# Kernel optimization log

Measured on AMD Instinct MI355X. Metric: run time of the kernel, lower is better.

Reference implementation:

```python
import jax, jax.numpy as jnp
import numpy as np

D = 768
B, T = 4, 4096


def _layernorm(x, gamma, bias):
    # Faithful to the (buggy) original: (x - mu/sqrt(var)) * gamma + bias,
    # with torch's default unbiased variance (ddof=1).
    mu = jnp.mean(x, axis=-1, keepdims=True)
    var = jnp.var(x, axis=-1, keepdims=True, ddof=1)
    return (x - mu / jnp.sqrt(var)) * gamma + bias


def setup_inputs() -> dict:
    key = jax.random.key(0)
    ks = jax.random.split(key, 8)
    # kaiming_uniform_ default: bound = sqrt(6 / fan_in) with a=sqrt(5) -> gain = sqrt(2/(1+5)) = sqrt(1/3)
    # bound = gain * sqrt(3/fan_in) = sqrt(1/fan_in)
    bound_attn = 1.0 / np.sqrt(D)
    bound_lin = 1.0 / np.sqrt(D)  # torch Linear default init bound
    return {
        "x": jax.random.normal(ks[0], (B, T, D), dtype=jnp.float32),
        "ln1_g": jnp.ones((D,), jnp.float32),
        "ln1_b": jnp.zeros((D,), jnp.float32),
        "wq": jax.random.uniform(ks[1], (D, D), jnp.float32, -bound_attn, bound_attn),
        "wk": jax.random.uniform(ks[2], (D, D), jnp.float32, -bound_attn, bound_attn),
        "wv": jax.random.uniform(ks[3], (D, D), jnp.float32, -bound_attn, bound_attn),
        "ln2_g": jnp.ones((D,), jnp.float32),
        "ln2_b": jnp.zeros((D,), jnp.float32),
        "fc1_w": jax.random.uniform(ks[4], (D, D), jnp.float32, -bound_lin, bound_lin),
        "fc1_b": jax.random.uniform(ks[5], (D,), jnp.float32, -bound_lin, bound_lin),
        "fc2_w": jax.random.uniform(ks[6], (D, D), jnp.float32, -bound_lin, bound_lin),
        "fc2_b": jax.random.uniform(ks[7], (D,), jnp.float32, -bound_lin, bound_lin),
    }


def reference(x, ln1_g, ln1_b, wq, wk, wv, ln2_g, ln2_b, fc1_w, fc1_b, fc2_w, fc2_b):
    d_model = x.shape[-1]
    # LN 1
    y = _layernorm(x, ln1_g, ln1_b)
    # Naive single-head attention (no causal mask, scale 1/sqrt(d_model))
    q = jnp.einsum("btk,kd->btd", y, wq)
    k = jnp.einsum("btk,kd->btd", y, wk)
    v = jnp.einsum("btk,kd->btd", y, wv)
    scale = 1.0 / jnp.sqrt(jnp.asarray(d_model, y.dtype))
    a = jax.nn.softmax(jnp.einsum("bqd,bkd->bqk", q, k) * scale, axis=-1)
    y = jnp.einsum("bqt,btd->bqd", a, v)
    # LN 2
    y = _layernorm(y, ln2_g, ln2_b)
    # MLP: Linear -> ReLU -> Linear (Dropout in eval mode = identity)
    h = jax.nn.relu(jnp.einsum("btd,od->bto", y, fc1_w) + fc1_b)
    y = jnp.einsum("btd,od->bto", h, fc2_w) + fc2_b
    # Residual
    return x + y
```

## Files before the change

kernel.cpp:

```cpp
#include <hip/hip_runtime.h>
#include <hip/hip_bf16.h>


#define DDIM 768
#define TT   4096
#define NB   4
#define ROWS (NB * TT)

using bf16 = __hip_bfloat16;
typedef __bf16 bf16x8 __attribute__((ext_vector_type(8)));
typedef float  f32x4  __attribute__((ext_vector_type(4)));
typedef unsigned short us4 __attribute__((ext_vector_type(4)));

__device__ __forceinline__ float to_f(float x) { return x; }
__device__ __forceinline__ float to_f(bf16 x) { return __bfloat162float(x); }

__device__ __forceinline__ unsigned short bfb(float f) {
  bf16 b = __float2bfloat16(f);
  return __builtin_bit_cast(unsigned short, b);
}

__device__ __forceinline__ void gload16(const void* g, void* l) {
#if __has_builtin(__builtin_amdgcn_global_load_lds)
  __builtin_amdgcn_global_load_lds(
      (const __attribute__((address_space(1))) void*)g,
      (__attribute__((address_space(3))) void*)l, 16, 0, 0);
#else
  int lane = threadIdx.x & 63;
  ((int4*)l)[lane] = *(const int4*)g;
#endif
}

#define SBAR()                                        \
  do {                                                \
    __builtin_amdgcn_sched_barrier(0);                \
    asm volatile("s_barrier" ::: "memory");           \
    __builtin_amdgcn_sched_barrier(0);                \
  } while (0)
#define VMW8() asm volatile("s_waitcnt vmcnt(8)" ::: "memory")
#define VMW0() asm volatile("s_waitcnt vmcnt(0)" ::: "memory")

template <int IH, int JH>
__device__ __forceinline__ void mmaQ(f32x4 (&acc)[8][4],
                                     const bf16x8 (&af)[4][2],
                                     const bf16x8 (&bfh)[2][2]) {
  __builtin_amdgcn_s_setprio(1);
#pragma unroll
  for (int ii = 0; ii < 4; ++ii)
#pragma unroll
    for (int jj = 0; jj < 2; ++jj)
#pragma unroll
      for (int kk = 0; kk < 2; ++kk)
        acc[IH * 4 + ii][JH * 2 + jj] = __builtin_amdgcn_mfma_f32_16x16x32_bf16(
            af[ii][kk], bfh[jj][kk], acc[IH * 4 + ii][JH * 2 + jj], 0, 0, 0);
  __builtin_amdgcn_s_setprio(0);
}

__global__ __launch_bounds__(512) void gemm_qk8(
    const bf16* __restrict__ A, int lda, long sA,
    const bf16* __restrict__ B, int ldb, long sB,
    bf16* __restrict__ Pout, int ldc, long sC, int K, float scale,
    float* __restrict__ Lsum) {
  __shared__ __align__(16) bf16 As[2][256 * 64];
  __shared__ __align__(16) bf16 Bs[2][256 * 64];

  const int h   = blockIdx.x;
  const int xcd = h & 7;
  const int s   = h >> 3;
  const int bx  = s % 16;
  const int g   = (s / 16) * 8 + xcd;
  const int by  = g % 16;
  const int bz  = g / 16;

  const char* Ab = (const char*)(A + (long)bz * sA);
  const char* Bb = (const char*)(B + (long)bz * sB);

  const int tid  = threadIdx.x;
  const int wave = tid >> 6;
  const int lane = tid & 63;
  const int l16  = lane & 15;
  const int lq   = lane >> 4;
  const int wm   = wave >> 2;
  const int wn   = wave & 3;
  const long tileM = (long)by * 256;
  const long tileN = (long)bx * 256;

  const int  pu  = wave * 1024 + lane * 16;
  const int  r0  = pu >> 7;
  const int  cc0 = (pu & 127) ^ ((r0 & 7) << 4);
  const long aoff   = (tileM + r0) * (long)lda * 2 + cc0;
  const long boff   = (tileN + r0) * (long)ldb * 2 + cc0;
  const long arow64 = 64 * (long)lda * 2;
  const long brow64 = 64 * (long)ldb * 2;
  char* As0 = (char*)As[0];
  char* As1 = (char*)As[1];
  char* Bs0 = (char*)Bs[0];
  char* Bs1 = (char*)Bs[1];
  const int ldst = wave * 1024;

  auto stageA = [&](char* dst, int t) {
    const long kb = (long)t * 128;
    gload16(Ab + aoff + kb,               dst + ldst);
    gload16(Ab + aoff + arow64 + kb,      dst + 8192 + ldst);
    gload16(Ab + aoff + 2 * arow64 + kb,  dst + 16384 + ldst);
    gload16(Ab + aoff + 3 * arow64 + kb,  dst + 24576 + ldst);
  };
  auto stageB = [&](char* dst, int t) {
    const long kb = (long)t * 128;
    gload16(Bb + boff + kb,               dst + ldst);
    gload16(Bb + boff + brow64 + kb,      dst + 8192 + ldst);
    gload16(Bb + boff + 2 * brow64 + kb,  dst + 16384 + ldst);
    gload16(Bb + boff + 3 * brow64 + kb,  dst + 24576 + ldst);
  };

  const int sw = (l16 & 7) << 4;
  auto rdA = [&](const char* buf, int ih, bf16x8 (&af)[4][2]) {
#pragma unroll
    for (int ii = 0; ii < 4; ++ii)
#pragma unroll
      for (int kk = 0; kk < 2; ++kk)
        af[ii][kk] = *(const bf16x8*)(buf +
            (wm * 128 + ih * 64 + ii * 16 + l16) * 128 +
            ((kk * 64 + lq * 16) ^ sw));
  };
  auto rdB = [&](const char* buf, int jh, bf16x8 (&bfh)[2][2]) {
#pragma unroll
    for (int jj = 0; jj < 2; ++jj)
#pragma unroll
      for (int kk = 0; kk < 2; ++kk)
        bfh[jj][kk] = *(const bf16x8*)(buf +
            (wn * 64 + (jh * 2 + jj) * 16 + l16) * 128 +
            ((kk * 64 + lq * 16) ^ sw));
  };

  f32x4 acc[8][4] = {};
  bf16x8 af[4][2], bf0[2][2], bf1[2][2];

  stageA(As0, 0);
  stageB(Bs0, 0);
  stageA(As1, 1);

  const int NI = K / 128;
  for (int I = 0; I < NI; ++I) {
    const int a = 2 * I, b = 2 * I + 1;
    const bool last = (I == NI - 1);

    stageB(Bs1, b);
    VMW8();
    SBAR();
    rdA(As0, 0, af);
    rdB(Bs0, 0, bf0);
    mmaQ<0, 0>(acc, af, bf0);
    SBAR();
    rdB(Bs0, 1, bf1);
    SBAR();
    mmaQ<0, 1>(acc, af, bf1);
    SBAR();
    rdA(As0, 1, af);
    SBAR();
    mmaQ<1, 1>(acc, af, bf1);
    SBAR();
    if (!last) stageA(As0, a + 2);
    SBAR();
    mmaQ<1, 0>(acc, af, bf0);
    SBAR();

    if (!last) {
      stageB(Bs0, a + 2);
      VMW8();
    } else {
      VMW0();
    }
    SBAR();
    rdA(As1, 0, af);
    rdB(Bs1, 0, bf0);
    mmaQ<0, 0>(acc, af, bf0);
    SBAR();
    rdB(Bs1, 1, bf1);
    SBAR();
    mmaQ<0, 1>(acc, af, bf1);
    SBAR();
    rdA(As1, 1, af);
    SBAR();
    mmaQ<1, 1>(acc, af, bf1);
    SBAR();
    if (!last) stageA(As1, b + 2);
    SBAR();
    mmaQ<1, 0>(acc, af, bf0);
    SBAR();
  }

  float* Lred = (float*)As0;
  const long base_k = tileM + wm * 128;
  const long base_q = tileN + wn * 64;
  bf16* P = Pout + (long)bz * sC;
  float ps[4] = {0.f, 0.f, 0.f, 0.f};
#pragma unroll
  for (int j = 0; j < 4; ++j) {
    const long colq = base_q + j * 16 + l16;
#pragma unroll
    for (int i = 0; i < 8; ++i) {
      const long krow = base_k + i * 16 + lq * 4;
      const float p0 = exp2f(acc[i][j][0] * scale);
      const float p1 = exp2f(acc[i][j][1] * scale);
      const float p2 = exp2f(acc[i][j][2] * scale);
      const float p3 = exp2f(acc[i][j][3] * scale);
      ps[j] += (p0 + p1) + (p2 + p3);
      us4 w = {bfb(p0), bfb(p1), bfb(p2), bfb(p3)};
      *(us4*)(P + colq * (long)ldc + krow) = w;
    }
  }
  if (tid < 256) Lred[tid] = 0.f;
  __syncthreads();
#pragma unroll
  for (int j = 0; j < 4; ++j) {
    float v = ps[j];
    v += __shfl_xor(v, 16);
    v += __shfl_xor(v, 32);
    if (lq == 0) atomicAdd(&Lred[wn * 64 + j * 16 + l16], v);
  }
  __syncthreads();
  if (tid < 256) atomicAdd(&Lsum[(long)bz * TT + tileN + tid], Lred[tid]);
}

template <int MODE, int SWZ, int NT, int MT>
__global__ __launch_bounds__(256) void gemm_bt(
    const bf16* __restrict__ A, int lda, long sA,
    const bf16* __restrict__ B, int ldb, long sB,
    void* __restrict__ Cout, int ldc, long sC, int K, float scale,
    const float* __restrict__ bias, const float* __restrict__ resid,
    float* __restrict__ Lsum) {
  __shared__ __align__(16) bf16 As[128 * 64];
  __shared__ __align__(16) bf16 Bs[128 * 64];

  int bx, by, bz;
  if constexpr (SWZ == 1) {
    const int h   = blockIdx.x;
    const int xcd = h & 7;
    const int s   = h >> 3;
    bx = s % NT;
    const int g = (s / NT) * 8 + xcd;
    by = g % MT;
    bz = g / MT;
  } else if constexpr (SWZ == 2) {
    const int h   = blockIdx.x;
    const int xcd = h & 7;
    const int s   = h >> 3;
    by = s % MT;
    const int g = (s / MT) * 8 + xcd;
    bx = g % NT;
    bz = g / NT;
  } else {
    bx = blockIdx.x; by = blockIdx.y; bz = blockIdx.z;
  }

  int kz = 0;
  if constexpr (MODE == 7) { kz = bz >> 2; bz &= 3; }

  A += (long)bz * sA + (long)kz * 2048;
  B += (long)bz * sB + (long)kz * 2048;

  const int tid  = threadIdx.x;
  const int wave = tid >> 6;
  const int lane = tid & 63;
  const int l16  = lane & 15;
  const int lq   = lane >> 4;
  const int wm   = wave >> 1;
  const int wn   = wave & 1;
  const long tileM = (long)by * 128;
  const long tileN = (long)bx * 128;

  f32x4 acc[4][4] = {};

  unsigned int aoff[4], boff[4];
#pragma unroll
  for (int q = 0; q < 4; ++q) {
    const int p    = (q * 4 + wave) * 1024 + lane * 16;
    const int lg   = p ^ (((p >> 7) & 7) << 4);
    const int row  = lg >> 7;
    const int colb = lg & 127;
    aoff[q] = (unsigned int)((tileM + row) * (long)lda * 2 + colb);
    boff[q] = (unsigned int)((tileN + row) * (long)ldb * 2 + colb);
  }

  const char* Ab = (const char*)A;
  const char* Bb = (const char*)B;
  char* AsB = (char*)As;
  char* BsB = (char*)Bs;
  const int sw = (l16 & 7) << 4;

  for (int kb = 0; kb < K * 2; kb += 128) {
#pragma unroll
    for (int q = 0; q < 4; ++q)
      gload16(Ab + (aoff[q] + kb), AsB + (q * 4 + wave) * 1024);
#pragma unroll
    for (int q = 0; q < 4; ++q)
      gload16(Bb + (boff[q] + kb), BsB + (q * 4 + wave) * 1024);
    __syncthreads();

#pragma unroll
    for (int kk = 0; kk < 2; ++kk) {
      bf16x8 af[4], bf_[4];
      const int ks = (kk * 64 + lq * 16) ^ sw;
#pragma unroll
      for (int i = 0; i < 4; ++i)
        af[i] = *(const bf16x8*)(AsB + (wm * 64 + i * 16 + l16) * 128 + ks);
#pragma unroll
      for (int j = 0; j < 4; ++j)
        bf_[j] = *(const bf16x8*)(BsB + (wn * 64 + j * 16 + l16) * 128 + ks);
#pragma unroll
      for (int i = 0; i < 4; ++i)
#pragma unroll
        for (int j = 0; j < 4; ++j)
          acc[i][j] = __builtin_amdgcn_mfma_f32_16x16x32_bf16(af[i], bf_[j],
                                                              acc[i][j], 0, 0, 0);
    }
    __syncthreads();
  }

  const long base_m = tileM + wm * 64;
  const long base_n = tileN + wn * 64;

  if constexpr (MODE == 7) {
    bf16* Op = (bf16*)Cout + (long)kz * ((long)ROWS * DDIM) + (long)bz * sC;
#pragma unroll
    for (int j = 0; j < 4; ++j) {
      const long colq = base_n + j * 16 + l16;
#pragma unroll
      for (int i = 0; i < 4; ++i) {
        const long drow = base_m + i * 16 + lq * 4;
        us4 w = {bfb(acc[i][j][0]), bfb(acc[i][j][1]),
                 bfb(acc[i][j][2]), bfb(acc[i][j][3])};
        *(us4*)(Op + colq * (long)ldc + drow) = w;
      }
    }
  } else if constexpr (MODE == 3) {
    bf16* Hp = (bf16*)Cout;
#pragma unroll
    for (int i = 0; i < 4; ++i) {
      const long drow = base_m + i * 16 + lq * 4;
      const f32x4 bv = *(const f32x4*)&bias[drow];
#pragma unroll
      for (int j = 0; j < 4; ++j) {
        const long colt = base_n + j * 16 + l16;
        float v0 = acc[i][j][0] + bv[0]; v0 = v0 > 0.f ? v0 : 0.f;
        float v1 = acc[i][j][1] + bv[1]; v1 = v1 > 0.f ? v1 : 0.f;
        float v2 = acc[i][j][2] + bv[2]; v2 = v2 > 0.f ? v2 : 0.f;
        float v3 = acc[i][j][3] + bv[3]; v3 = v3 > 0.f ? v3 : 0.f;
        us4 w = {bfb(v0), bfb(v1), bfb(v2), bfb(v3)};
        *(us4*)(Hp + colt * (long)ldc + drow) = w;
      }
    }
  } else {
    float* Op = (float*)Cout;
#pragma unroll
    for (int i = 0; i < 4; ++i) {
      const long drow = base_m + i * 16 + lq * 4;
      const f32x4 bv = *(const f32x4*)&bias[drow];
#pragma unroll
      for (int j = 0; j < 4; ++j) {
        const long off = (base_n + j * 16 + l16) * (long)ldc + drow;
        const f32x4 rs = *(const f32x4*)&resid[off];
        f32x4 o;
        o[0] = acc[i][j][0] + bv[0] + rs[0];
        o[1] = acc[i][j][1] + bv[1] + rs[1];
        o[2] = acc[i][j][2] + bv[2] + rs[2];
        o[3] = acc[i][j][3] + bv[3] + rs[3];
        __builtin_nontemporal_store(o, (f32x4*)(Op + off));
      }
    }
  }
}

__global__ __launch_bounds__(256) void gemm_qkv(
    const bf16* __restrict__ Y,
    const bf16* __restrict__ Wq, const bf16* __restrict__ Wk,
    const bf16* __restrict__ Wv, bf16* __restrict__ Qm,
    bf16* __restrict__ Km, bf16* __restrict__ Vt) {
  __shared__ __align__(16) bf16 As[128 * 64];
  __shared__ __align__(16) bf16 Bs[128 * 64];

  const int z = blockIdx.z;
  const bf16* Ap = (z == 2) ? Wv : Y;
  const bf16* Bp = (z == 0) ? Wq : (z == 1) ? Wk : Y;

  const int tid  = threadIdx.x;
  const int wave = tid >> 6;
  const int lane = tid & 63;
  const int l16  = lane & 15;
  const int lq   = lane >> 4;
  const int wm   = wave >> 1;
  const int wn   = wave & 1;
  const long tileM = (z == 2) ? (long)blockIdx.x * 128 : (long)blockIdx.y * 128;
  const long tileN = (z == 2) ? (long)blockIdx.y * 128 : (long)blockIdx.x * 128;

  unsigned int aoff[4], boff[4];
#pragma unroll
  for (int q = 0; q < 4; ++q) {
    const int p    = (q * 4 + wave) * 1024 + lane * 16;
    const int lg   = p ^ (((p >> 7) & 7) << 4);
    const int row  = lg >> 7;
    const int colb = lg & 127;
    aoff[q] = (unsigned int)((tileM + row) * (long)DDIM * 2 + colb);
    boff[q] = (unsigned int)((tileN + row) * (long)DDIM * 2 + colb);
  }

  f32x4 acc[4][4] = {};

  const char* Ab = (const char*)Ap;
  const char* Bb = (const char*)Bp;
  char* AsB = (char*)As;
  char* BsB = (char*)Bs;
  const int sw = (l16 & 7) << 4;

  for (int kb = 0; kb < DDIM * 2; kb += 128) {
#pragma unroll
    for (int q = 0; q < 4; ++q)
      gload16(Ab + (aoff[q] + kb), AsB + (q * 4 + wave) * 1024);
#pragma unroll
    for (int q = 0; q < 4; ++q)
      gload16(Bb + (boff[q] + kb), BsB + (q * 4 + wave) * 1024);
    __syncthreads();

#pragma unroll
    for (int kk = 0; kk < 2; ++kk) {
      bf16x8 af[4], bf_[4];
      const int ks = (kk * 64 + lq * 16) ^ sw;
#pragma unroll
      for (int i = 0; i < 4; ++i)
        af[i] = *(const bf16x8*)(AsB + (wm * 64 + i * 16 + l16) * 128 + ks);
#pragma unroll
      for (int j = 0; j < 4; ++j)
        bf_[j] = *(const bf16x8*)(BsB + (wn * 64 + j * 16 + l16) * 128 + ks);
#pragma unroll
      for (int i = 0; i < 4; ++i)
#pragma unroll
        for (int j = 0; j < 4; ++j)
          acc[i][j] = __builtin_amdgcn_mfma_f32_16x16x32_bf16(af[i], bf_[j],
                                                              acc[i][j], 0, 0, 0);
    }
    __syncthreads();
  }

  const long base_m = tileM + wm * 64;
  const long base_n = tileN + wn * 64;
  bf16* Cp = (z == 0) ? Qm : (z == 1) ? Km : Vt;
  const long ldo = (z < 2) ? (long)DDIM : (long)ROWS;
#pragma unroll
  for (int i = 0; i < 4; ++i)
#pragma unroll
    for (int j = 0; j < 4; ++j)
#pragma unroll
      for (int r = 0; r < 4; ++r) {
        const long row = base_m + i * 16 + lq * 4 + r;
        const long col = base_n + j * 16 + l16;
        Cp[row * ldo + col] = __float2bfloat16(acc[i][j][r]);
      }
}

template <typename T, int DUAL>
__global__ __launch_bounds__(256) void ln_kernel(
    const T* __restrict__ in, const T* __restrict__ in2,
    const float* __restrict__ Ldiv, const float* __restrict__ g,
    const float* __restrict__ beta, bf16* __restrict__ out,
    float* __restrict__ Lzero) {
  const long row = blockIdx.x;
  if (Lzero != nullptr && threadIdx.x == 0) Lzero[row] = 0.f;
  const T* xr = in + row * DDIM;
  const int t = threadIdx.x;
  float v0 = to_f(xr[t]), v1 = to_f(xr[t + 256]), v2 = to_f(xr[t + 512]);
  if constexpr (DUAL) {
    const T* xr2 = in2 + row * DDIM;
    v0 += to_f(xr2[t]); v1 += to_f(xr2[t + 256]); v2 += to_f(xr2[t + 512]);
    const float invL = 1.0f / Ldiv[row];
    v0 *= invL; v1 *= invL; v2 *= invL;
  }
  float s = v0 + v1 + v2;
  float q = v0 * v0 + v1 * v1 + v2 * v2;
#pragma unroll
  for (int o = 32; o; o >>= 1) {
    s += __shfl_down(s, o);
    q += __shfl_down(q, o);
  }
  __shared__ float sb[4], qb[4];
  if ((t & 63) == 0) { sb[t >> 6] = s; qb[t >> 6] = q; }
  __syncthreads();
  const float S = sb[0] + sb[1] + sb[2] + sb[3];
  const float Q = qb[0] + qb[1] + qb[2] + qb[3];
  const float mu  = S * (1.0f / 768.0f);
  const float var = (Q - 768.0f * mu * mu) * (1.0f / 767.0f);
  const float sub = mu / sqrtf(var);
  bf16* orow = out + row * DDIM;
  orow[t]       = __float2bfloat16((v0 - sub) * g[t]       + beta[t]);
  orow[t + 256] = __float2bfloat16((v1 - sub) * g[t + 256] + beta[t + 256]);
  orow[t + 512] = __float2bfloat16((v2 - sub) * g[t + 512] + beta[t + 512]);
}

__global__ void prep_weights(const float* __restrict__ wq,
                             const float* __restrict__ wk,
                             const float* __restrict__ wv,
                             const float* __restrict__ f1,
                             const float* __restrict__ f2,
                             bf16* wqt, bf16* wkt, bf16* wvt, bf16* f1b,
                             bf16* f2b) {
  __shared__ float tile[32][33];
  const float* src;
  bf16* dst;
  bool tr = true;
  switch (blockIdx.z) {
    case 0: src = wq; dst = wqt; break;
    case 1: src = wk; dst = wkt; break;
    case 2: src = wv; dst = wvt; break;
    case 3: src = f1; dst = f1b; tr = false; break;
    default: src = f2; dst = f2b; tr = false; break;
  }
  const int tx = threadIdx.x, ty = threadIdx.y;
  const int x = blockIdx.x * 32 + tx;
  const int y = blockIdx.y * 32 + ty;
  if (tr) {
#pragma unroll
    for (int r = 0; r < 4; ++r) tile[ty + 8 * r][tx] = src[(y + 8 * r) * DDIM + x];
    __syncthreads();
    const int ox = blockIdx.y * 32 + tx;
    const int oy = blockIdx.x * 32 + ty;
#pragma unroll
    for (int r = 0; r < 4; ++r)
      dst[(oy + 8 * r) * DDIM + ox] = __float2bfloat16(tile[tx][ty + 8 * r]);
  } else {
#pragma unroll
    for (int r = 0; r < 4; ++r)
      dst[(y + 8 * r) * DDIM + x] = __float2bfloat16(src[(y + 8 * r) * DDIM + x]);
  }
}

extern "C" void kernel_launch(void* const* d_in, const int* in_sizes, int n_in,
                              void* d_out, int out_size, void* d_ws,
                              size_t ws_size, hipStream_t stream) {
  const float* x     = (const float*)d_in[0];
  const float* ln1_g = (const float*)d_in[1];
  const float* ln1_b = (const float*)d_in[2];
  const float* wq    = (const float*)d_in[3];
  const float* wk    = (const float*)d_in[4];
  const float* wv    = (const float*)d_in[5];
  const float* ln2_g = (const float*)d_in[6];
  const float* ln2_b = (const float*)d_in[7];
  const float* f1w   = (const float*)d_in[8];
  const float* f1bias= (const float*)d_in[9];
  const float* f2w   = (const float*)d_in[10];
  const float* f2bias= (const float*)d_in[11];
  float* out = (float*)d_out;

  char* ws = (char*)d_ws;
  size_t off = 0;
  auto take = [&](size_t bytes) -> char* {
    char* p = ws + off;
    off += (bytes + 255) & ~(size_t)255;
    return p;
  };
  const size_t WB = (size_t)DDIM * DDIM * sizeof(bf16);
  const size_t MB = (size_t)ROWS * DDIM * sizeof(bf16);
  bf16* wqt = (bf16*)take(WB);
  bf16* wkt = (bf16*)take(WB);
  bf16* wvt = (bf16*)take(WB);
  bf16* f1b = (bf16*)take(WB);
  bf16* f2b = (bf16*)take(WB);
  float* Lsum = (float*)take((size_t)ROWS * sizeof(float));
  bf16* y1  = (bf16*)take(MB);
  bf16* Qm  = (bf16*)take(MB);
  bf16* Km  = (bf16*)take(MB);
  bf16* Vt  = (bf16*)take(MB);
  bf16* Sb  = (bf16*)take((size_t)NB * TT * TT * sizeof(bf16));
  bf16* O0 = y1;
  bf16* O1 = Qm;
  bf16* y2 = Km;
  bf16* h  = y1;

  prep_weights<<<dim3(24, 24, 5), dim3(32, 8), 0, stream>>>(
      wq, wk, wv, f1w, f2w, wqt, wkt, wvt, f1b, f2b);

  ln_kernel<float, 0><<<ROWS, 256, 0, stream>>>(x, nullptr, nullptr, ln1_g,
                                                ln1_b, y1, Lsum);

  gemm_qkv<<<dim3(6, 128, 3), 256, 0, stream>>>(y1, wqt, wkt, wvt, Qm, Km, Vt);

  const float scale2 = 0.03608439182435161f * 1.4426950408889634f;
  gemm_qk8<<<dim3(16 * 16 * NB), 512, 0, stream>>>(
      Km, DDIM, (long)TT * DDIM, Qm, DDIM, (long)TT * DDIM, Sb, TT,
      (long)TT * TT, DDIM, scale2, Lsum);

  gemm_bt<7, 2, 32, 6><<<dim3(6 * 32 * NB * 2), 256, 0, stream>>>(
      Vt, ROWS, (long)TT, Sb, TT, (long)TT * TT, O0, DDIM, (long)TT * DDIM,
      TT / 2, 1.f, nullptr, nullptr, nullptr);

  ln_kernel<bf16, 1><<<ROWS, 256, 0, stream>>>(O0, O1, Lsum, ln2_g, ln2_b, y2,
                                               nullptr);

  gemm_bt<3, 2, 128, 6><<<dim3(128 * 6), 256, 0, stream>>>(
      f1b, DDIM, 0, y2, DDIM, 0, h, DDIM, 0, DDIM, 1.f, f1bias, nullptr,
      nullptr);
  gemm_bt<4, 2, 128, 6><<<dim3(128 * 6), 256, 0, stream>>>(
      f2b, DDIM, 0, h, DDIM, 0, out, DDIM, 0, DDIM, 1.f, f2bias, x, nullptr);
}
```

Before: 549.8 us.

## Interleave per-row global-to-LDS loads across MFMA phases in GEMM main loop

Splits each 4-load A/B tile staging into single-row loads and spreads them between the MFMA quadrant phases of the double-buffered loop. The vmcnt wait drops from 8 to 3 to match the finer-grained issue. The goal is to smooth memory traffic and hide global load latency behind matrix math rather than issuing bursts of loads. The tighter wait counts make correctness depend on the exact load ordering, and the extra bounds checks in each load add a little overhead.

```diff
diff --git a/kernel.cpp b/kernel.cpp
--- a/kernel.cpp
+++ b/kernel.cpp
@@ -37,7 +37,7 @@
     asm volatile("s_barrier" ::: "memory");           \
     __builtin_amdgcn_sched_barrier(0);                \
   } while (0)
-#define VMW8() asm volatile("s_waitcnt vmcnt(8)" ::: "memory")
+#define VMW3() asm volatile("s_waitcnt vmcnt(3)" ::: "memory")
 #define VMW0() asm volatile("s_waitcnt vmcnt(0)" ::: "memory")
 
 template <int IH, int JH>
@@ -98,19 +98,18 @@
   char* Bs1 = (char*)Bs[1];
   const int ldst = wave * 1024;
 
-  auto stageA = [&](char* dst, int t) {
-    const long kb = (long)t * 128;
-    gload16(Ab + aoff + kb,               dst + ldst);
-    gload16(Ab + aoff + arow64 + kb,      dst + 8192 + ldst);
-    gload16(Ab + aoff + 2 * arow64 + kb,  dst + 16384 + ldst);
-    gload16(Ab + aoff + 3 * arow64 + kb,  dst + 24576 + ldst);
+  const int NT = K / 64;
+  const int NI = K / 128;
+
+  auto stA = [&](char* dst, int t, int u) {
+    if (t < NT)
+      gload16(Ab + aoff + (long)t * 128 + (long)u * arow64,
+              dst + u * 8192 + ldst);
   };
-  auto stageB = [&](char* dst, int t) {
-    const long kb = (long)t * 128;
-    gload16(Bb + boff + kb,               dst + ldst);
-    gload16(Bb + boff + brow64 + kb,      dst + 8192 + ldst);
-    gload16(Bb + boff + 2 * brow64 + kb,  dst + 16384 + ldst);
-    gload16(Bb + boff + 3 * brow64 + kb,  dst + 24576 + ldst);
+  auto stB = [&](char* dst, int t, int u) {
+    if (t < NT)
+      gload16(Bb + boff + (long)t * 128 + (long)u * brow64,
+              dst + u * 8192 + ldst);
   };
 
   const int sw = (l16 & 7) << 4;
@@ -136,55 +135,54 @@
   f32x4 acc[8][4] = {};
   bf16x8 af[4][2], bf0[2][2], bf1[2][2];
 
-  stageA(As0, 0);
-  stageB(Bs0, 0);
-  stageA(As1, 1);
-
-  const int NI = K / 128;
+  stA(As0, 0, 0); stA(As0, 0, 1); stA(As0, 0, 2); stA(As0, 0, 3);
+  stB(Bs0, 0, 0); stB(Bs0, 0, 1); stB(Bs0, 0, 2); stB(Bs0, 0, 3);
+  stA(As1, 1, 0);
+
   for (int I = 0; I < NI; ++I) {
-    const int a = 2 * I, b = 2 * I + 1;
+    const int b = 2 * I + 1, a2 = 2 * I + 2, b2 = 2 * I + 3;
     const bool last = (I == NI - 1);
 
-    stageB(Bs1, b);
-    VMW8();
+    stA(As1, b, 1); stB(Bs1, b, 0);
+    VMW3();
     SBAR();
     rdA(As0, 0, af);
     rdB(Bs0, 0, bf0);
     mmaQ<0, 0>(acc, af, bf0);
     SBAR();
+    stA(As1, b, 2); stB(Bs1, b, 1);
     rdB(Bs0, 1, bf1);
     SBAR();
     mmaQ<0, 1>(acc, af, bf1);
     SBAR();
+    stA(As1, b, 3); stB(Bs1, b, 2);
     rdA(As0, 1, af);
     SBAR();
     mmaQ<1, 1>(acc, af, bf1);
     SBAR();
-    if (!last) stageA(As0, a + 2);
+    stB(Bs1, b, 3); stA(As0, a2, 0);
     SBAR();
     mmaQ<1, 0>(acc, af, bf0);
     SBAR();
 
-    if (!last) {
-      stageB(Bs0, a + 2);
-      VMW8();
-    } else {
-      VMW0();
-    }
+    stA(As0, a2, 1); stB(Bs0, a2, 0);
+    if (last) { VMW0(); } else { VMW3(); }
     SBAR();
     rdA(As1, 0, af);
     rdB(Bs1, 0, bf0);
     mmaQ<0, 0>(acc, af, bf0);
     SBAR();
+    stA(As0, a2, 2); stB(Bs0, a2, 1);
     rdB(Bs1, 1, bf1);
     SBAR();
     mmaQ<0, 1>(acc, af, bf1);
     SBAR();
+    stA(As0, a2, 3); stB(Bs0, a2, 2);
     rdA(As1, 1, af);
     SBAR();
     mmaQ<1, 1>(acc, af, bf1);
     SBAR();
-    if (!last) stageA(As1, b + 2);
+    stB(Bs0, a2, 3); stA(As1, b2, 0);
     SBAR();
     mmaQ<1, 0>(acc, af, bf0);
     SBAR();
```

After: 546.4 us. No clear change (-0.6%).
